# Performance work log

Measured on AMD Instinct MI355X. Metric: run time of the kernel, lower is better.

The kernel has to match this reference:

```python
import jax, jax.numpy as jnp
import numpy as np

VOCAB, EMB, HID = 32000, 512, 512
B, S = 4, 2048


def _log_g(x):
    # log of g(x) where g(x) = x + 0.5 for x >= 0 else sigmoid(x)
    return jnp.where(x >= 0, jnp.log(jax.nn.relu(x) + 0.5), -jax.nn.softplus(-x))


def _layernorm(x, gamma, beta, eps):
    mu = jnp.mean(x, axis=-1, keepdims=True)
    var = jnp.mean(jnp.square(x - mu), axis=-1, keepdims=True)
    return (x - mu) * jax.lax.rsqrt(var + eps) * gamma + beta


def _mingru_layer(x, W):
    # x: [B,S,D_in], W: [D_in, 2*H] (no bias for minGRU)
    k, h_pre = jnp.split(x @ W, 2, axis=-1)          # gate pre-act, candidate pre-act
    log_coeffs = -jax.nn.softplus(k)                 # log(1 - z)
    log_b = -jax.nn.softplus(-k) + _log_g(h_pre)     # log(z) + log(g(h~))
    # Heinsen log-domain parallel scan along time axis
    a_star = jnp.cumsum(log_coeffs, axis=1)          # [B,S,H]
    log_h = a_star + jax.lax.cumlogsumexp(log_b - a_star, axis=1)
    return jnp.exp(log_h)


def setup_inputs() -> dict:
    key = jax.random.key(0)
    ks = jax.random.split(key, 8)
    s = 0.02
    return {
        "ids": jax.random.randint(ks[0], (B, S), 0, VOCAB, dtype=jnp.int32),
        "emb": jax.random.normal(ks[1], (VOCAB, EMB), jnp.float32) * s,
        "W0": jax.random.normal(ks[2], (EMB, 2 * HID), jnp.float32) * s,
        "W1": jax.random.normal(ks[3], (HID, 2 * HID), jnp.float32) * s,
        "ln0_g": jnp.ones((EMB,), jnp.float32),
        "ln0_b": jnp.zeros((EMB,), jnp.float32),
        "ln1_g": jnp.ones((HID,), jnp.float32),
        "ln1_b": jnp.zeros((HID,), jnp.float32),
        "lnf_g": jnp.ones((HID,), jnp.float32),
        "lnf_b": jnp.zeros((HID,), jnp.float32),
        "fc_w": jax.random.normal(ks[4], (HID, VOCAB), jnp.float32) * s,
        "fc_b": jnp.zeros((VOCAB,), jnp.float32),
    }


def reference(ids, emb, W0, W1, ln0_g, ln0_b, ln1_g, ln1_b, lnf_g, lnf_b, fc_w, fc_b):
    x = emb[ids]  # [B,S,EMB]
    for W, g, b in ((W0, ln0_g, ln0_b), (W1, ln1_g, ln1_b)):
        inp = x
        xn = _layernorm(x, g, b, 1e-5)           # pre-layer norm (cfg['norm']=True)
        x = _mingru_layer(xn, W) + inp           # residual=True, dropout=0
    x = _layernorm(x, lnf_g, lnf_b, 0.0)         # torch code passes bias as eps -> eps=0.0
    logits = x @ fc_w + fc_b                     # [B,S,VOCAB]
    return logits
```

## Files before the change

### kernel.cpp

```cpp
#include <hip/hip_runtime.h>

typedef __attribute__((ext_vector_type(8))) short short8;
typedef __attribute__((ext_vector_type(4))) float f32x4;
typedef __attribute__((ext_vector_type(8))) unsigned short u16x8;

#define B_ 4
#define S_ 2048
#define EMB_ 512
#define HID_ 512
#define VOCAB_ 32000
#define ROWS (B_ * S_)
#define NCHUNK 32
#define CHUNK 64

#define FK_ 512
#define NBN_F 125
#define OT_PER_BLK 16
#define NBLK_F (NBN_F * 2)
#define NT_TOT (OT_PER_BLK * 8)
#define EP_OFF 131072
#define BIAS_OFF (EP_OFF + 20480)
#define SMEM_TOT (BIAS_OFF + 1024)

__device__ __forceinline__ unsigned short f2bf(float f) {
    unsigned int u = __float_as_uint(f);
    u += 0x7fffu + ((u >> 16) & 1u);
    return (unsigned short)(u >> 16);
}

__device__ __forceinline__ void gl_lds16(const unsigned short* g, unsigned short* l) {
    __builtin_amdgcn_global_load_lds(
        (const __attribute__((address_space(1))) unsigned int*)(uintptr_t)(g),
        (__attribute__((address_space(3))) unsigned int*)(unsigned int)(uintptr_t)(l),
        16, 0, 0);
}

__global__ __launch_bounds__(256) void transpose_convert_k(
    const float* __restrict__ src, unsigned short* __restrict__ dst, int K, int N) {
    __shared__ float t[32][33];
    int kt = blockIdx.y * 32, nt = blockIdx.x * 32;
    int tx = threadIdx.x & 31, ty = threadIdx.x >> 5;
#pragma unroll
    for (int i = 0; i < 4; i++)
        t[ty + i * 8][tx] = src[(size_t)(kt + ty + i * 8) * N + nt + tx];
    __syncthreads();
#pragma unroll
    for (int i = 0; i < 4; i++)
        dst[(size_t)(nt + ty + i * 8) * K + kt + tx] = f2bf(t[tx][ty + i * 8]);
}

__global__ __launch_bounds__(256) void prep_k(
    const int* __restrict__ ids, const float* __restrict__ emb,
    const float* __restrict__ gam, const float* __restrict__ bet,
    float* __restrict__ xres, unsigned short* __restrict__ xw,
    const float* __restrict__ W0, unsigned short* __restrict__ wt0,
    const float* __restrict__ W1, unsigned short* __restrict__ wt1,
    const float* __restrict__ fcw, unsigned short* __restrict__ fcwt) {
    __shared__ float t[32][33];
    int vb = blockIdx.x;
    int tid = threadIdx.x;
    if (vb < 2048) {
        int row = vb * 4 + (tid >> 6);
        int lane = tid & 63;
        const float4* src = (const float4*)(emb + (size_t)ids[row] * EMB_);
        float v[8];
        *(float4*)(v) = src[lane * 2];
        *(float4*)(v + 4) = src[lane * 2 + 1];
        float s = 0.f, s2 = 0.f;
#pragma unroll
        for (int j = 0; j < 8; j++) { s += v[j]; s2 += v[j] * v[j]; }
#pragma unroll
        for (int off = 1; off < 64; off <<= 1) {
            s += __shfl_xor(s, off);
            s2 += __shfl_xor(s2, off);
        }
        float mu = s * (1.f / EMB_);
        float var = fmaxf(s2 * (1.f / EMB_) - mu * mu, 0.f);
        float rstd = rsqrtf(var + 1e-5f);
        float4* xr = (float4*)(xres + (size_t)row * EMB_);
        xr[lane * 2] = *(float4*)(v);
        xr[lane * 2 + 1] = *(float4*)(v + 4);
        u16x8 o;
#pragma unroll
        for (int j = 0; j < 8; j++) {
            int c = lane * 8 + j;
            o[j] = f2bf((v[j] - mu) * rstd * gam[c] + bet[c]);
        }
        *(u16x8*)(xw + (size_t)row * EMB_ + lane * 8) = o;
        return;
    }
    vb -= 2048;
    const float* src;
    unsigned short* dst;
    int N;
    if (vb < 512)        { src = W0;  dst = wt0;  N = 1024; }
    else if (vb < 1024)  { vb -= 512;  src = W1;  dst = wt1;  N = 1024; }
    else                 { vb -= 1024; src = fcw; dst = fcwt; N = VOCAB_; }
    int ntiles = N >> 5;
    int ktile = vb / ntiles, ntile = vb - ktile * ntiles;
    int kt = ktile << 5, nt = ntile << 5;
    int tx = tid & 31, ty = tid >> 5;
#pragma unroll
    for (int i = 0; i < 4; i++)
        t[ty + i * 8][tx] = src[(size_t)(kt + ty + i * 8) * N + nt + tx];
    __syncthreads();
#pragma unroll
    for (int i = 0; i < 4; i++)
        dst[(size_t)(nt + ty + i * 8) * 512 + kt + tx] = f2bf(t[tx][ty + i * 8]);
}

__global__ __launch_bounds__(256) void ln_k(
    const float* __restrict__ xsrc,
    const float* __restrict__ gam, const float* __restrict__ bet,
    unsigned short* __restrict__ xw, float eps) {
    int row = blockIdx.x * 4 + (threadIdx.x >> 6);
    int lane = threadIdx.x & 63;
    const float4* src = (const float4*)(xsrc + (size_t)row * HID_);
    float v[8];
    *(float4*)(v) = src[lane * 2];
    *(float4*)(v + 4) = src[lane * 2 + 1];
    float s = 0.f, s2 = 0.f;
#pragma unroll
    for (int j = 0; j < 8; j++) { s += v[j]; s2 += v[j] * v[j]; }
#pragma unroll
    for (int off = 1; off < 64; off <<= 1) {
        s += __shfl_xor(s, off);
        s2 += __shfl_xor(s2, off);
    }
    float mu = s * (1.f / HID_);
    float var = fmaxf(s2 * (1.f / HID_) - mu * mu, 0.f);
    float rstd = rsqrtf(var + eps);
    u16x8 o;
#pragma unroll
    for (int j = 0; j < 8; j++) {
        int c = lane * 8 + j;
        o[j] = f2bf((v[j] - mu) * rstd * gam[c] + bet[c]);
    }
    *(u16x8*)(xw + (size_t)row * HID_ + lane * 8) = o;
}

__global__ __launch_bounds__(256) void gemm_bf16_k(
    const unsigned short* __restrict__ A, const unsigned short* __restrict__ Bt,
    float* __restrict__ C, int M, int N, int K) {
    __shared__ unsigned short lA[128 * 64];
    __shared__ unsigned short lB[128 * 64];
    __shared__ float eT[4][16 * 68];
    int tid = threadIdx.x;
    int w = tid >> 6, l = tid & 63;
    int m0 = blockIdx.y * 128, n0 = blockIdx.x * 128;
    int wm = w >> 1, wn = w & 1;
    f32x4 acc[4][4] = {};

    int rIn = l >> 3;
    int cOff = (l & 7) * 8;

    for (int k0 = 0; k0 < K; k0 += 64) {
#pragma unroll
        for (int i = 0; i < 4; i++) {
            int c = w * 4 + i;
            gl_lds16(A + (size_t)(m0 + c * 8 + rIn) * K + k0 + cOff, &lA[c * 512]);
            gl_lds16(Bt + (size_t)(n0 + c * 8 + rIn) * K + k0 + cOff, &lB[c * 512]);
        }
        asm volatile("s_waitcnt vmcnt(0)" ::: "memory");
        __syncthreads();

        const unsigned short* pa = lA + ((size_t)(wm * 64 + (l & 15)) * 64) + ((l >> 4) * 8);
        const unsigned short* pb = lB + ((size_t)(wn * 64 + (l & 15)) * 64) + ((l >> 4) * 8);
#pragma unroll
        for (int kk = 0; kk < 2; kk++) {
            short8 af[4], bfr[4];
#pragma unroll
            for (int m = 0; m < 4; m++) af[m] = *(const short8*)(pa + m * 16 * 64 + kk * 32);
#pragma unroll
            for (int n = 0; n < 4; n++) bfr[n] = *(const short8*)(pb + n * 16 * 64 + kk * 32);
#pragma unroll
            for (int m = 0; m < 4; m++)
#pragma unroll
                for (int n = 0; n < 4; n++)
                    acc[m][n] = __builtin_amdgcn_mfma_f32_16x16x32_bf16(af[m], bfr[n], acc[m][n], 0, 0, 0);
        }
        __syncthreads();
    }

    float* ep = eT[w];
    int rl = l >> 4, slot = l & 15;
    int rbase = m0 + wm * 64, cbase = n0 + wn * 64;
#pragma unroll
    for (int mf = 0; mf < 4; ++mf) {
#pragma unroll
        for (int nf = 0; nf < 4; ++nf)
#pragma unroll
            for (int j = 0; j < 4; ++j)
                ep[(rl * 4 + j) * 68 + nf * 16 + slot] = acc[mf][nf][j];
        asm volatile("s_waitcnt lgkmcnt(0)" ::: "memory");
#pragma unroll
        for (int p = 0; p < 4; ++p) {
            int r = p * 4 + rl;
            f32x4 vv = *(const f32x4*)(ep + r * 68 + slot * 4);
            *(f32x4*)(C + (size_t)(rbase + mf * 16 + r) * N + cbase + slot * 4) = vv;
        }
        asm volatile("s_waitcnt lgkmcnt(0)" ::: "memory");
    }
}

__device__ __forceinline__ void stageP(
    const unsigned short* __restrict__ A, const unsigned short* __restrict__ Bt,
    int bmbase, int bn, int H, char* smem, int r0, int c0, unsigned wq) {
    if (H >= 4 * NT_TOT) return;
    int T = H >> 2, j = H & 3;
    int ti = T >> 3, kt = T & 7;
    const unsigned short* src = (j < 2) ? A : Bt;
    int row0 = ((j < 2) ? ((bmbase + ti) << 8) : (bn << 8)) + ((j & 1) << 7);
    unsigned tb = ((unsigned)(T & 1) << 16) | ((unsigned)(j >> 1) << 15) | ((unsigned)(j & 1) << 14);
    const unsigned short* g0 = src + (size_t)(row0 + r0) * FK_ + ((kt << 6) + c0);
    gl_lds16(g0, (unsigned short*)(smem + tb + wq));
    gl_lds16(g0 + (size_t)64 * FK_, (unsigned short*)(smem + tb + 8192 + wq));
}

#define MIDBAR() __builtin_amdgcn_s_barrier()
#define ENDBAR() do { asm volatile("s_waitcnt lgkmcnt(0)" ::: "memory"); \
                      asm volatile("s_barrier" ::: "memory"); } while (0)

#define PHASE_MFMA(AF, BF, MO, NO)                                                  \
    do {                                                                            \
        __builtin_amdgcn_s_setprio(1);                                             \
        _Pragma("unroll") for (int mf = 0; mf < 4; ++mf)                            \
        _Pragma("unroll") for (int nf = 0; nf < 2; ++nf)                            \
        _Pragma("unroll") for (int ks = 0; ks < 2; ++ks)                            \
            acc[(MO) + mf][(NO) + nf] = __builtin_amdgcn_mfma_f32_16x16x32_bf16(    \
                AF[mf][ks], BF[nf][ks], acc[(MO) + mf][(NO) + nf], 0, 0, 0);        \
        __builtin_amdgcn_s_setprio(0);                                             \
    } while (0)

__global__ __launch_bounds__(512, 2) void gemmP_k(
    const unsigned short* __restrict__ A, const unsigned short* __restrict__ Bt,
    const float* __restrict__ bias, float* __restrict__ C) {
    extern __shared__ char smem[];
    int tid = threadIdx.x;
    int w = tid >> 6, l = tid & 63;
    int wm = w >> 2, wn = w & 3;

    int bn = blockIdx.x % NBN_F;
    int bmbase = (blockIdx.x / NBN_F) * OT_PER_BLK;

    int r0 = ((w >> 1) << 4) + (l >> 2);
    int c0 = ((w & 1) << 5) + (((l & 3) << 3) ^ ((l & 32) ? 16 : 0));
    unsigned wq = (unsigned)(w << 10);

    unsigned rowpart = (unsigned)(((l & 15) << 6) + (((((l >> 4) << 3)) ^ ((l & 8) ? 16 : 0)) << 1));
    unsigned aoff = ((unsigned)wm << 14) + rowpart;
    unsigned boff = 32768u + ((unsigned)wn << 13) + rowpart;

    f32x4 acc[8][4] = {};

    if (tid < 64) {
        f32x4 bv = *(const f32x4*)(bias + (bn << 8) + (tid << 2));
        *(f32x4*)(smem + BIAS_OFF + (tid << 4)) = bv;
    }
    asm volatile("s_waitcnt vmcnt(0) lgkmcnt(0)" ::: "memory");
    asm volatile("" ::: "memory");

    stageP(A, Bt, bmbase, bn, 0, smem, r0, c0, wq); asm volatile("" ::: "memory");
    stageP(A, Bt, bmbase, bn, 1, smem, r0, c0, wq); asm volatile("" ::: "memory");
    stageP(A, Bt, bmbase, bn, 2, smem, r0, c0, wq); asm volatile("" ::: "memory");
    stageP(A, Bt, bmbase, bn, 3, smem, r0, c0, wq); asm volatile("" ::: "memory");
    stageP(A, Bt, bmbase, bn, 4, smem, r0, c0, wq); asm volatile("" ::: "memory");
    stageP(A, Bt, bmbase, bn, 5, smem, r0, c0, wq);
    asm volatile("s_waitcnt vmcnt(4)" ::: "memory");
    asm volatile("s_barrier" ::: "memory");

    for (int T = 0; T < NT_TOT; ++T) {
        const char* pA = smem + (((unsigned)(T & 1)) << 16) + aoff;
        const char* pB = smem + (((unsigned)(T & 1)) << 16) + boff;
        short8 A0[4][2], A1[4][2], B0[2][2], B1[2][2];

#pragma unroll
        for (int mf = 0; mf < 4; ++mf)
#pragma unroll
            for (int ks = 0; ks < 2; ++ks)
                A0[mf][ks] = *(const short8*)(pA + mf * 2048 + ks * 1024);
#pragma unroll
        for (int nf = 0; nf < 2; ++nf)
#pragma unroll
            for (int ks = 0; ks < 2; ++ks)
                B0[nf][ks] = *(const short8*)(pB + nf * 2048 + ks * 1024);
        stageP(A, Bt, bmbase, bn, 4 * T + 6, smem, r0, c0, wq);
        MIDBAR();
        PHASE_MFMA(A0, B0, 0, 0);
        ENDBAR();

#pragma unroll
        for (int mf = 0; mf < 4; ++mf)
#pragma unroll
            for (int ks = 0; ks < 2; ++ks)
                A1[mf][ks] = *(const short8*)(pA + (4 + mf) * 2048 + ks * 1024);
#pragma unroll
        for (int nf = 0; nf < 2; ++nf)
#pragma unroll
            for (int ks = 0; ks < 2; ++ks)
                B1[nf][ks] = *(const short8*)(pB + (2 + nf) * 2048 + ks * 1024);
        stageP(A, Bt, bmbase, bn, 4 * T + 7, smem, r0, c0, wq);
        MIDBAR();
        PHASE_MFMA(A1, B0, 4, 0);
        ENDBAR();

        stageP(A, Bt, bmbase, bn, 4 * T + 8, smem, r0, c0, wq);
        MIDBAR();
        PHASE_MFMA(A1, B1, 4, 2);
        ENDBAR();

        stageP(A, Bt, bmbase, bn, 4 * T + 9, smem, r0, c0, wq);
        if (T < NT_TOT - 2)       { asm volatile("s_waitcnt vmcnt(4)" ::: "memory"); }
        else if (T == NT_TOT - 2) { asm volatile("s_waitcnt vmcnt(0)" ::: "memory"); }
        MIDBAR();
        PHASE_MFMA(A0, B1, 0, 2);
        ENDBAR();

        if ((T & 7) == 7) {
            int bm = bmbase + (T >> 3);
            float* ep = (float*)(smem + EP_OFF) + w * (16 * 40);
            const float* bls = (const float*)(smem + BIAS_OFF);
            int rl = l >> 4, slot = l & 15;
            int rbase = (bm << 8) + (wm << 7);
            int cbase = (bn << 8) + (wn << 6);
            float bs[4];
#pragma unroll
            for (int nf = 0; nf < 4; ++nf) bs[nf] = bls[(wn << 6) + nf * 16 + slot];
#pragma unroll
            for (int mf = 0; mf < 8; ++mf) {
#pragma unroll
                for (int nfp = 0; nfp < 2; ++nfp) {
#pragma unroll
                    for (int nf2 = 0; nf2 < 2; ++nf2)
#pragma unroll
                        for (int j = 0; j < 4; ++j)
                            ep[(rl * 4 + j) * 40 + nf2 * 16 + slot] =
                                acc[mf][nfp * 2 + nf2][j] + bs[nfp * 2 + nf2];
                    asm volatile("s_waitcnt lgkmcnt(0)" ::: "memory");
#pragma unroll
                    for (int p = 0; p < 2; ++p) {
                        int r = p * 8 + (l >> 3);
                        f32x4 vv = *(const f32x4*)(ep + r * 40 + (l & 7) * 4);
                        __builtin_nontemporal_store(vv,
                            (f32x4*)(C + (size_t)(rbase + mf * 16 + r) * VOCAB_ +
                                     cbase + nfp * 32 + (l & 7) * 4));
                    }
                    asm volatile("s_waitcnt lgkmcnt(0)" ::: "memory");
                }
#pragma unroll
                for (int nf = 0; nf < 4; ++nf) acc[mf][nf] = f32x4{0.f, 0.f, 0.f, 0.f};
            }
        }
    }
}

__device__ __forceinline__ void gate_terms(float k, float hp, float& a, float& b) {
    float z = 1.f / (1.f + __expf(-k));
    a = 1.f - z;
    float g = (hp >= 0.f) ? (hp + 0.5f) : (1.f / (1.f + __expf(-hp)));
    b = z * g;
}

__global__ __launch_bounds__(256) void scan1_k(
    const float* __restrict__ proj, float* __restrict__ Ach, float* __restrict__ Bch) {
    int t = blockIdx.x * 256 + threadIdx.x;
    int h = t & (HID_ - 1);
    int bc = t >> 9;
    int b = bc >> 5, c = bc & (NCHUNK - 1);
    const float* p = proj + ((size_t)(b * S_ + c * CHUNK)) * (2 * HID_) + h;
    float A = 1.f, H = 0.f;
#pragma unroll 4
    for (int s = 0; s < CHUNK; s++) {
        float k = p[(size_t)s * (2 * HID_)];
        float hp = p[(size_t)s * (2 * HID_) + HID_];
        float a, bb;
        gate_terms(k, hp, a, bb);
        H = a * H + bb;
        A *= a;
    }
    Ach[t] = A;
    Bch[t] = H;
}

__global__ __launch_bounds__(256) void scan23_k(
    const float* __restrict__ proj, const float* __restrict__ Ach,
    const float* __restrict__ Bch, float* __restrict__ xres) {
    int t = blockIdx.x * 256 + threadIdx.x;
    int h = t & (HID_ - 1);
    int bc = t >> 9;
    int b = bc >> 5, c = bc & (NCHUNK - 1);
    float H = 0.f;
    for (int cp = 0; cp < c; cp++) {
        int idx = (b * NCHUNK + cp) * HID_ + h;
        H = Ach[idx] * H + Bch[idx];
    }
    const float* p = proj + ((size_t)(b * S_ + c * CHUNK)) * (2 * HID_) + h;
    float* x = xres + ((size_t)(b * S_ + c * CHUNK)) * HID_ + h;
#pragma unroll 4
    for (int s = 0; s < CHUNK; s++) {
        float k = p[(size_t)s * (2 * HID_)];
        float hp = p[(size_t)s * (2 * HID_) + HID_];
        float a, bb;
        gate_terms(k, hp, a, bb);
        H = a * H + bb;
        x[(size_t)s * HID_] += H;
    }
}

extern "C" void kernel_launch(void* const* d_in, const int* in_sizes, int n_in,
                              void* d_out, int out_size, void* d_ws, size_t ws_size,
                              hipStream_t stream) {
    const int* ids = (const int*)d_in[0];
    const float* emb = (const float*)d_in[1];
    const float* W0 = (const float*)d_in[2];
    const float* W1 = (const float*)d_in[3];
    const float* ln0_g = (const float*)d_in[4];
    const float* ln0_b = (const float*)d_in[5];
    const float* ln1_g = (const float*)d_in[6];
    const float* ln1_b = (const float*)d_in[7];
    const float* lnf_g = (const float*)d_in[8];
    const float* lnf_b = (const float*)d_in[9];
    const float* fc_w = (const float*)d_in[10];
    const float* fc_b = (const float*)d_in[11];
    float* out = (float*)d_out;

    (void)hipFuncSetAttribute((const void*)gemmP_k,
                              hipFuncAttributeMaxDynamicSharedMemorySize, SMEM_TOT);

    char* ws = (char*)d_ws;
    const size_t OFF_XW   = 0;
    const size_t OFF_PROJ = 8388608;
    const size_t OFF_XRES = OFF_PROJ + 33554432;
    const size_t OFF_WT0  = OFF_XRES + 16777216;
    const size_t OFF_WT1  = OFF_WT0 + 1048576;
    const size_t OFF_SA   = OFF_WT1 + 1048576;
    const size_t OFF_SB   = OFF_SA + 262144;
    const size_t OFF_FCWT = OFF_SB + 262144;
    const size_t NEED_BIG = OFF_FCWT + 32768000;

    unsigned short* xw  = (unsigned short*)(ws + OFF_XW);
    float* proj         = (float*)(ws + OFF_PROJ);
    float* xres         = (float*)(ws + OFF_XRES);
    unsigned short* wt0 = (unsigned short*)(ws + OFF_WT0);
    unsigned short* wt1 = (unsigned short*)(ws + OFF_WT1);
    float* sA = (float*)(ws + OFF_SA);
    float* sB = (float*)(ws + OFF_SB);

    bool big = ws_size >= NEED_BIG;
    unsigned short* fcwt = big ? (unsigned short*)(ws + OFF_FCWT)
                               : (unsigned short*)(ws + OFF_PROJ);

    if (big) {
        prep_k<<<2048 + 1024 + 16000, 256, 0, stream>>>(
            ids, emb, ln0_g, ln0_b, xres, xw, W0, wt0, W1, wt1, fc_w, fcwt);
    } else {
        prep_k<<<2048 + 1024, 256, 0, stream>>>(
            ids, emb, ln0_g, ln0_b, xres, xw, W0, wt0, W1, wt1, fc_w, wt0);
    }

    gemm_bf16_k<<<dim3(1024 / 128, ROWS / 128), 256, 0, stream>>>(xw, wt0, proj, ROWS, 1024, 512);
    scan1_k<<<65536 / 256, 256, 0, stream>>>(proj, sA, sB);
    scan23_k<<<65536 / 256, 256, 0, stream>>>(proj, sA, sB, xres);

    ln_k<<<ROWS / 4, 256, 0, stream>>>(xres, ln1_g, ln1_b, xw, 1e-5f);
    gemm_bf16_k<<<dim3(1024 / 128, ROWS / 128), 256, 0, stream>>>(xw, wt1, proj, ROWS, 1024, 512);
    scan1_k<<<65536 / 256, 256, 0, stream>>>(proj, sA, sB);
    scan23_k<<<65536 / 256, 256, 0, stream>>>(proj, sA, sB, xres);

    ln_k<<<ROWS / 4, 256, 0, stream>>>(xres, lnf_g, lnf_b, xw, 0.0f);
    if (!big) {
        transpose_convert_k<<<dim3(VOCAB_ / 32, 512 / 32), 256, 0, stream>>>(fc_w, fcwt, 512, VOCAB_);
    }
    gemmP_k<<<NBLK_F, 512, SMEM_TOT, stream>>>(xw, fcwt, fc_b, out);
}
```

Before: 537.0 us.

## Fuse scan second pass with layernorm and shrink scan chunks to 16

Merges the chunked-scan finalize pass with the following layernorm into one kernel, where each 512-thread block owns one chunk of 16 timesteps and computes row statistics via wave shuffles plus shared-memory reduction. This avoids writing and re-reading the residual stream between the scan and the norm, and skips the final residual write entirely. The chunk count rises from 32 to 128 per batch for more parallelism. The cost is a longer serial carry-in loop over prior chunks and a block-wide barrier per timestep.

```diff
diff --git a/kernel.cpp b/kernel.cpp
--- a/kernel.cpp
+++ b/kernel.cpp
@@ -10,8 +10,8 @@
 #define HID_ 512
 #define VOCAB_ 32000
 #define ROWS (B_ * S_)
-#define NCHUNK 32
-#define CHUNK 64
+#define NCHUNK 128
+#define CHUNK 16
 
 #define FK_ 512
 #define NBN_F 125
@@ -109,36 +109,6 @@
         dst[(size_t)(nt + ty + i * 8) * 512 + kt + tx] = f2bf(t[tx][ty + i * 8]);
 }
 
-__global__ __launch_bounds__(256) void ln_k(
-    const float* __restrict__ xsrc,
-    const float* __restrict__ gam, const float* __restrict__ bet,
-    unsigned short* __restrict__ xw, float eps) {
-    int row = blockIdx.x * 4 + (threadIdx.x >> 6);
-    int lane = threadIdx.x & 63;
-    const float4* src = (const float4*)(xsrc + (size_t)row * HID_);
-    float v[8];
-    *(float4*)(v) = src[lane * 2];
-    *(float4*)(v + 4) = src[lane * 2 + 1];
-    float s = 0.f, s2 = 0.f;
-#pragma unroll
-    for (int j = 0; j < 8; j++) { s += v[j]; s2 += v[j] * v[j]; }
-#pragma unroll
-    for (int off = 1; off < 64; off <<= 1) {
-        s += __shfl_xor(s, off);
-        s2 += __shfl_xor(s2, off);
-    }
-    float mu = s * (1.f / HID_);
-    float var = fmaxf(s2 * (1.f / HID_) - mu * mu, 0.f);
-    float rstd = rsqrtf(var + eps);
-    u16x8 o;
-#pragma unroll
-    for (int j = 0; j < 8; j++) {
-        int c = lane * 8 + j;
-        o[j] = f2bf((v[j] - mu) * rstd * gam[c] + bet[c]);
-    }
-    *(u16x8*)(xw + (size_t)row * HID_ + lane * 8) = o;
-}
-
 __global__ __launch_bounds__(256) void gemm_bf16_k(
     const unsigned short* __restrict__ A, const unsigned short* __restrict__ Bt,
     float* __restrict__ C, int M, int N, int K) {
@@ -366,10 +336,10 @@
     int t = blockIdx.x * 256 + threadIdx.x;
     int h = t & (HID_ - 1);
     int bc = t >> 9;
-    int b = bc >> 5, c = bc & (NCHUNK - 1);
+    int b = bc >> 7, c = bc & (NCHUNK - 1);
     const float* p = proj + ((size_t)(b * S_ + c * CHUNK)) * (2 * HID_) + h;
     float A = 1.f, H = 0.f;
-#pragma unroll 4
+#pragma unroll
     for (int s = 0; s < CHUNK; s++) {
         float k = p[(size_t)s * (2 * HID_)];
         float hp = p[(size_t)s * (2 * HID_) + HID_];
@@ -382,28 +352,61 @@
     Bch[t] = H;
 }
 
-__global__ __launch_bounds__(256) void scan23_k(
+__global__ __launch_bounds__(512) void scanln_k(
     const float* __restrict__ proj, const float* __restrict__ Ach,
-    const float* __restrict__ Bch, float* __restrict__ xres) {
-    int t = blockIdx.x * 256 + threadIdx.x;
-    int h = t & (HID_ - 1);
-    int bc = t >> 9;
-    int b = bc >> 5, c = bc & (NCHUNK - 1);
+    const float* __restrict__ Bch, float* __restrict__ xres,
+    const float* __restrict__ gam, const float* __restrict__ bet,
+    unsigned short* __restrict__ xw, float eps, int write_xres) {
+    __shared__ float redS[2][8], redQ[2][8];
+    int bc = blockIdx.x;
+    int b = bc >> 7, c = bc & (NCHUNK - 1);
+    int h = threadIdx.x;
+    int w = h >> 6, l = h & 63;
+
     float H = 0.f;
     for (int cp = 0; cp < c; cp++) {
         int idx = (b * NCHUNK + cp) * HID_ + h;
         H = Ach[idx] * H + Bch[idx];
     }
+
     const float* p = proj + ((size_t)(b * S_ + c * CHUNK)) * (2 * HID_) + h;
-    float* x = xres + ((size_t)(b * S_ + c * CHUNK)) * HID_ + h;
-#pragma unroll 4
+    float* xr = xres + ((size_t)(b * S_ + c * CHUNK)) * HID_ + h;
+    float Hs[CHUNK];
+#pragma unroll
     for (int s = 0; s < CHUNK; s++) {
         float k = p[(size_t)s * (2 * HID_)];
         float hp = p[(size_t)s * (2 * HID_) + HID_];
         float a, bb;
         gate_terms(k, hp, a, bb);
         H = a * H + bb;
-        x[(size_t)s * HID_] += H;
+        Hs[s] = H + xr[(size_t)s * HID_];
+    }
+    if (write_xres) {
+#pragma unroll
+        for (int s = 0; s < CHUNK; s++) xr[(size_t)s * HID_] = Hs[s];
+    }
+
+    float g = gam[h], be = bet[h];
+    unsigned short* xwp = xw + ((size_t)(b * S_ + c * CHUNK)) * HID_ + h;
+#pragma unroll 1
+    for (int s = 0; s < CHUNK; s++) {
+        float v = Hs[s];
+        float sm = v, sq = v * v;
+#pragma unroll
+        for (int off = 1; off < 64; off <<= 1) {
+            sm += __shfl_xor(sm, off);
+            sq += __shfl_xor(sq, off);
+        }
+        int par = s & 1;
+        if (l == 0) { redS[par][w] = sm; redQ[par][w] = sq; }
+        __syncthreads();
+        float S = 0.f, Q = 0.f;
+#pragma unroll
+        for (int i = 0; i < 8; i++) { S += redS[par][i]; Q += redQ[par][i]; }
+        float mu = S * (1.f / HID_);
+        float var = fmaxf(Q * (1.f / HID_) - mu * mu, 0.f);
+        float rstd = rsqrtf(var + eps);
+        xwp[(size_t)s * HID_] = f2bf((v - mu) * rstd * g + be);
     }
 }
 
@@ -434,8 +437,8 @@
     const size_t OFF_WT0  = OFF_XRES + 16777216;
     const size_t OFF_WT1  = OFF_WT0 + 1048576;
     const size_t OFF_SA   = OFF_WT1 + 1048576;
-    const size_t OFF_SB   = OFF_SA + 262144;
-    const size_t OFF_FCWT = OFF_SB + 262144;
+    const size_t OFF_SB   = OFF_SA + 1048576;
+    const size_t OFF_FCWT = OFF_SB + 1048576;
     const size_t NEED_BIG = OFF_FCWT + 32768000;
 
     unsigned short* xw  = (unsigned short*)(ws + OFF_XW);
@@ -459,15 +462,13 @@
     }
 
     gemm_bf16_k<<<dim3(1024 / 128, ROWS / 128), 256, 0, stream>>>(xw, wt0, proj, ROWS, 1024, 512);
-    scan1_k<<<65536 / 256, 256, 0, stream>>>(proj, sA, sB);
-    scan23_k<<<65536 / 256, 256, 0, stream>>>(proj, sA, sB, xres);
-
-    ln_k<<<ROWS / 4, 256, 0, stream>>>(xres, ln1_g, ln1_b, xw, 1e-5f);
+    scan1_k<<<262144 / 256, 256, 0, stream>>>(proj, sA, sB);
+    scanln_k<<<B_ * NCHUNK, 512, 0, stream>>>(proj, sA, sB, xres, ln1_g, ln1_b, xw, 1e-5f, 1);
+
     gemm_bf16_k<<<dim3(1024 / 128, ROWS / 128), 256, 0, stream>>>(xw, wt1, proj, ROWS, 1024, 512);
-    scan1_k<<<65536 / 256, 256, 0, stream>>>(proj, sA, sB);
-    scan23_k<<<65536 / 256, 256, 0, stream>>>(proj, sA, sB, xres);
-
-    ln_k<<<ROWS / 4, 256, 0, stream>>>(xres, lnf_g, lnf_b, xw, 0.0f);
+    scan1_k<<<262144 / 256, 256, 0, stream>>>(proj, sA, sB);
+    scanln_k<<<B_ * NCHUNK, 512, 0, stream>>>(proj, sA, sB, xres, lnf_g, lnf_b, xw, 0.0f, 0);
+
     if (!big) {
         transpose_convert_k<<<dim3(VOCAB_ / 32, 512 / 32), 256, 0, stream>>>(fc_w, fcwt, 512, VOCAB_);
     }
```

Result: no change. 541.6 us (+0.8%).
